# Kernel optimization log

Hardware: AMD Instinct MI355X
Metric: run time of the kernel (lower is better)

The kernel has to match this reference:

```python
import jax, jax.numpy as jnp
import numpy as np

B, T, RSS, L, FEAT, H = 256, 256, 12, 256, 8, 128
DIST_EPS = 1e-8
LN_EPS = 1e-5

def _lin(x, W, b):
    return x @ W.T + b

def setup_inputs() -> dict:
    key = jax.random.key(0)
    ks = jax.random.split(key, 20)
    w = lambda k, shape: jax.random.normal(k, shape, jnp.float32) * 0.1
    z = lambda *s: jnp.zeros(s, jnp.float32)
    # LED table: xyz positions in a room, frequency index in 1..12 (matches rss channels)
    pos = jax.random.uniform(ks[0], (L, 3), jnp.float32, 0.0, 5.0)
    freq = jax.random.randint(ks[1], (L,), 1, RSS + 1).astype(jnp.float32)
    return dict(
        rss_seq=jax.random.uniform(ks[2], (B, T, RSS), jnp.float32),
        global_led_pos_freq=jnp.concatenate([pos, freq[:, None]], axis=1),
        enc_W1=w(ks[3], (32, 4)), enc_b1=z(32), enc_W2=w(ks[4], (FEAT, 32)), enc_b2=z(FEAT),
        q_W1=w(ks[5], (64, 4)), q_b1=z(64), q_W2=w(ks[6], (64, 64)), q_b2=z(64),
        k_W1=w(ks[7], (64, FEAT + 3)), k_b1=z(64), k_W2=w(ks[8], (64, 64)), k_b2=z(64),
        Wih0=w(ks[9], (4 * H, RSS * (1 + FEAT))), Whh0=w(ks[10], (4 * H, H)), bih0=z(4 * H), bhh0=z(4 * H),
        Wih1=w(ks[11], (4 * H, H)), Whh1=w(ks[12], (4 * H, H)), bih1=z(4 * H), bhh1=z(4 * H),
        ln_g=jnp.ones((H,), jnp.float32), ln_b=z(H),
        fc_W1=w(ks[13], (H // 2, H)), fc_b1=z(H // 2), fc_W2=w(ks[14], (3, H // 2)), fc_b2=z(3),
    )

def _lstm_cell(x, h, c, Wih, Whh, bih, bhh):
    g = x @ Wih.T + bih + h @ Whh.T + bhh  # [B, 4H], pytorch gate order i,f,g,o
    i, f, gg, o = jnp.split(g, 4, axis=-1)
    c = jax.nn.sigmoid(f) * c + jax.nn.sigmoid(i) * jnp.tanh(gg)
    h = jax.nn.sigmoid(o) * jnp.tanh(c)
    return h, c

def _forward(rss_seq, global_led_pos_freq, enc_W1, enc_b1, enc_W2, enc_b2,
             q_W1, q_b1, q_W2, q_b2, k_W1, k_b1, k_W2, k_b2,
             Wih0, Whh0, bih0, bhh0, Wih1, Whh1, bih1, bhh1,
             ln_g, ln_b, fc_W1, fc_b1, fc_W2, fc_b2):
    batch, t_len, rss_dim = rss_seq.shape
    led_pos = global_led_pos_freq[:, :3]   # [L,3]
    led_freq = global_led_pos_freq[:, 3]   # [L]
    rss_freqs = jnp.arange(1, rss_dim + 1, dtype=rss_seq.dtype)
    freq_mask = rss_freqs[:, None] == led_freq[None, :]  # [RSS, L] bool
    # global LED features are a buffer computed under no_grad in torch
    led_feat = jax.lax.stop_gradient(
        jax.nn.relu(_lin(jax.nn.relu(_lin(global_led_pos_freq, enc_W1, enc_b1)), enc_W2, enc_b2)))  # [L,FEAT]
    keys = _lin(jax.nn.relu(_lin(jnp.concatenate([led_feat, led_pos], axis=1), k_W1, k_b1)), k_W2, k_b2)  # [L,64]
    neg = jnp.finfo(rss_seq.dtype).min

    def step(carry, rss_t):
        prev_pos, h0, c0, h1, c1 = carry  # prev_pos [B,3]
        q_in = jnp.concatenate(
            [rss_t[..., None], jnp.broadcast_to(prev_pos[:, None, :], (batch, rss_dim, 3))], axis=-1)  # [B,RSS,4]
        q = _lin(jax.nn.relu(_lin(q_in, q_W1, q_b1)), q_W2, q_b2)  # [B,RSS,64]
        scores = jnp.einsum('bqd,ld->bql', q, keys)  # [B,RSS,L]
        dist_sq = jnp.sum((prev_pos[:, None, :] - led_pos[None, :, :]) ** 2, axis=-1)  # [B,L]
        scores = scores + (-0.5 * jnp.log(dist_sq + DIST_EPS))[:, None, :]
        scores = jnp.where(freq_mask[None], scores, neg)
        attn = jax.nn.softmax(scores, axis=-1)
        agg = jnp.einsum('bql,lf->bqf', attn, led_feat)  # [B,RSS,FEAT]
        x = jnp.concatenate([rss_t[..., None], agg], axis=-1).reshape(batch, -1)  # [B, RSS*(1+FEAT)]
        h0n, c0n = _lstm_cell(x, h0, c0, Wih0, Whh0, bih0, bhh0)
        h1n, c1n = _lstm_cell(h0n, h1, c1, Wih1, Whh1, bih1, bhh1)
        y = h1n
        mu = jnp.mean(y, axis=-1, keepdims=True)
        var = jnp.var(y, axis=-1, keepdims=True)
        y = (y - mu) / jnp.sqrt(var + LN_EPS) * ln_g + ln_b
        pred = _lin(jax.nn.relu(_lin(y, fc_W1, fc_b1)), fc_W2, fc_b2)  # [B,3]
        return (pred, h0n, c0n, h1n, c1n), pred

    prev0 = jnp.broadcast_to(jnp.mean(led_pos, axis=0, keepdims=True), (batch, 3))
    hz = jnp.zeros((batch, Whh0.shape[1]), rss_seq.dtype)
    _, outs = jax.lax.scan(step, (prev0, hz, hz, hz, hz), jnp.swapaxes(rss_seq, 0, 1))
    return jnp.swapaxes(outs, 0, 1)  # [B,T,3]

def reference(rss_seq, global_led_pos_freq, enc_W1, enc_b1, enc_W2, enc_b2,
              q_W1, q_b1, q_W2, q_b2, k_W1, k_b1, k_W2, k_b2,
              Wih0, Whh0, bih0, bhh0, Wih1, Whh1, bih1, bhh1,
              ln_g, ln_b, fc_W1, fc_b1, fc_W2, fc_b2):
    return _forward(rss_seq, global_led_pos_freq, enc_W1, enc_b1, enc_W2, enc_b2,
                    q_W1, q_b1, q_W2, q_b2, k_W1, k_b1, k_W2, k_b2,
                    Wih0, Whh0, bih0, bhh0, Wih1, Whh1, bih1, bhh1,
                    ln_g, ln_b, fc_W1, fc_b1, fc_W2, fc_b2)
```

## Files before the change

kernel.cpp:

```cpp
#include <hip/hip_runtime.h>
#include <hip/hip_fp16.h>
#include <math.h>

#define B_ 256
#define T_ 256
#define RSS_ 12
#define L_ 256
#define FEAT_ 8
#define H_ 128

constexpr int OFF_PW0  = 0;
constexpr int OFF_PW1  = OFF_PW0 + 63488;
constexpr int OFF_W1L  = OFF_PW1 + 32768;
constexpr int OFF_B0   = OFF_W1L + 32768;
constexpr int OFF_B1   = OFF_B0 + 512;
constexpr int OFF_QW1T = OFF_B1 + 512;
constexpr int OFF_FC1  = OFF_QW1T + 256;
constexpr int OFF_K2T4 = OFF_FC1 + 8192;
constexpr int OFF_KB   = OFF_K2T4 + 16384;
constexpr int OFF_LF   = OFF_KB + 256;
constexpr int OFF_LPX  = OFF_LF + 2048;
constexpr int OFF_LPY  = OFF_LPX + 256;
constexpr int OFF_LPZ  = OFF_LPY + 256;
constexpr int OFF_MEAN = OFF_LPZ + 256;
constexpr int OFF_PREV0= OFF_MEAN + 8;
constexpr int OFF_INT  = OFF_PREV0 + 4;

__device__ __forceinline__ unsigned packh2(float a, float b) {
  const unsigned short lo = __half_as_ushort(__float2half(a));
  const unsigned short hi = __half_as_ushort(__float2half(b));
  return (unsigned)lo | ((unsigned)hi << 16);
}
__device__ __forceinline__ __half2 u2h2(unsigned u){ union { unsigned u; __half2 h; } c; c.u = u; return c.h; }
__device__ __forceinline__ float sigf(float x){ return 1.f/(1.f+expf(-x)); }

#if __has_builtin(__builtin_amdgcn_fdot2)
typedef _Float16 h2v __attribute__((ext_vector_type(2)));
__device__ __forceinline__ float d2(unsigned w, unsigned z, float acc) {
  union { unsigned u; h2v h; } cw, cz; cw.u = w; cz.u = z;
  return __builtin_amdgcn_fdot2(cw.h, cz.h, acc, false);
}
#else
__device__ __forceinline__ float d2(unsigned w, unsigned z, float acc) {
  const __half2 hw = u2h2(w), hz = u2h2(z);
  acc = fmaf(__low2float(hw),  __low2float(hz),  acc);
  return fmaf(__high2float(hw), __high2float(hz), acc);
}
#endif

constexpr int SZ_PW0 = 63488, SZ_PW1 = 32768, SZ_W1L = 32768, SZ_B = 512, SZ_Q = 256, SZ_FC = 8192;
constexpr int TOT_T = SZ_PW0 + SZ_PW1 + SZ_W1L + SZ_B + SZ_B + SZ_Q + SZ_FC;

__global__ void k_prep(const float* __restrict__ Wih0, const float* __restrict__ Whh0,
                       const float* __restrict__ bih0, const float* __restrict__ bhh0,
                       const float* __restrict__ Wih1, const float* __restrict__ Whh1,
                       const float* __restrict__ bih1, const float* __restrict__ bhh1,
                       const float* __restrict__ qW1,  const float* __restrict__ fcW1,
                       float* __restrict__ ws) {
  unsigned* wsu = (unsigned*)ws;
  for (int t = blockIdx.x*blockDim.x + threadIdx.x; t < TOT_T; t += gridDim.x*blockDim.x) {
    int u = t;
    if (u < SZ_PW0) {
      const int k = u & 3, j = (u >> 2) & 511, q = u >> 11;
      const int p = 4*q + k;
      float lo, hi;
      if (p < 60) {
        const int r = p / 5, e0 = 2*(p % 5), e1 = e0 + 1;
        lo = Wih0[j*108 + r*9 + e0];
        hi = (e1 <= 8) ? Wih0[j*108 + r*9 + e1] : 0.f;
      } else {
        const int i0 = 2*(p - 60);
        lo = Whh0[j*128 + i0]; hi = Whh0[j*128 + i0 + 1];
      }
      wsu[OFF_PW0 + u] = packh2(lo, hi); continue;
    } u -= SZ_PW0;
    if (u < SZ_PW1) {
      const int k = u & 3, j = (u >> 2) & 511, q = u >> 11;
      const int i0 = 2*(4*q + k);
      wsu[OFF_PW1 + u] = packh2(Wih1[j*128 + i0], Wih1[j*128 + i0 + 1]); continue;
    } u -= SZ_PW1;
    if (u < SZ_W1L) {
      const int k = u & 3, j = (u >> 2) & 511, q = u >> 11;
      const int i0 = 2*(4*q + k);
      wsu[OFF_W1L + u] = packh2(Whh1[j*128 + i0], Whh1[j*128 + i0 + 1]); continue;
    } u -= SZ_W1L;
    if (u < SZ_B) { ws[OFF_B0+u] = bih0[u]+bhh0[u]; continue; } u -= SZ_B;
    if (u < SZ_B) { ws[OFF_B1+u] = bih1[u]+bhh1[u]; continue; } u -= SZ_B;
    if (u < SZ_Q) { const int c=u>>6, j=u&63; ws[OFF_QW1T+u] = qW1[j*4+c]; continue; } u -= SZ_Q;
    { const int c = u >> 8, rem = u & 255, j = rem >> 2, k = rem & 3;
      ws[OFF_FC1 + u] = fcW1[j*128 + (c<<2) + k]; }
  }
}

__global__ __launch_bounds__(256) void k_led(const float* __restrict__ gplf,
    const float* __restrict__ encW1, const float* __restrict__ encb1,
    const float* __restrict__ encW2, const float* __restrict__ encb2,
    const float* __restrict__ kW1, const float* __restrict__ kb1,
    const float* __restrict__ kW2, const float* __restrict__ kb2,
    const float* __restrict__ qW2, const float* __restrict__ qb2,
    float* __restrict__ ws) {
  __shared__ float sLF[L_][FEAT_];
  __shared__ float sP[L_][3];
  __shared__ int   sR[L_];
  const int l = threadIdx.x;
  const float p0=gplf[l*4+0], p1=gplf[l*4+1], p2=gplf[l*4+2], fr=gplf[l*4+3];

  float e1[32];
  for (int j=0;j<32;++j) {
    float v = encb1[j] + encW1[j*4+0]*p0 + encW1[j*4+1]*p1 + encW1[j*4+2]*p2 + encW1[j*4+3]*fr;
    e1[j] = fmaxf(v,0.f);
  }
  float lf[8];
  for (int f=0;f<8;++f) {
    float v = encb2[f];
    for (int j=0;j<32;++j) v += encW2[f*32+j]*e1[j];
    lf[f] = fmaxf(v,0.f);
  }
  float kin[11] = {lf[0],lf[1],lf[2],lf[3],lf[4],lf[5],lf[6],lf[7],p0,p1,p2};
  float hh[64];
  for (int j=0;j<64;++j) {
    float v = kb1[j];
    for (int c=0;c<11;++c) v += kW1[j*11+c]*kin[c];
    hh[j]=fmaxf(v,0.f);
  }
  float kk[64];
  for (int d=0;d<64;++d) {
    float v = kb2[d];
    for (int j=0;j<64;++j) v += kW2[d*64+j]*hh[j];
    kk[d]=v;
  }
  float kbv=0.f;
  for (int d=0;d<64;++d) kbv += qb2[d]*kk[d];
  ws[OFF_KB+l]=kbv;
  for (int e=0;e<64;++e) {
    float acc=0.f;
    for (int d=0;d<64;++d) acc += qW2[d*64+e]*kk[d];
    ws[OFF_K2T4 + (e>>2)*1024 + l*4 + (e&3)] = acc;
  }
  for (int f=0;f<8;++f){ ws[OFF_LF+l*8+f]=lf[f]; sLF[l][f]=lf[f]; }
  ws[OFF_LPX+l]=p0; ws[OFF_LPY+l]=p1; ws[OFF_LPZ+l]=p2;
  sP[l][0]=p0; sP[l][1]=p1; sP[l][2]=p2;
  const int r = (int)fr - 1;
  sR[l]=r;
  int* iws = (int*)(ws + OFF_INT);
  iws[l] = r;
  __syncthreads();
  if (l==0) {
    int* cntp = iws + 256;
    int* idxp = cntp + 16;
    int c[12]; for (int r2=0;r2<12;++r2) c[r2]=0;
    for (int i=0;i<L_;++i){ int r2=sR[i]; idxp[r2*256 + c[r2]] = i; c[r2]++; }
    for (int r2=0;r2<12;++r2) cntp[r2]=c[r2];
    float mx=0.f,my=0.f,mz=0.f;
    for (int i=0;i<L_;++i){mx+=sP[i][0];my+=sP[i][1];mz+=sP[i][2];}
    ws[OFF_PREV0+0]=mx/(float)L_; ws[OFF_PREV0+1]=my/(float)L_; ws[OFF_PREV0+2]=mz/(float)L_;
    for (int f=0;f<8;++f){ float s=0.f; for (int i=0;i<L_;++i) s+=sLF[i][f]; ws[OFF_MEAN+f]=s/(float)L_; }
  }
}

__global__ __launch_bounds__(512,1) void k_main(const float* __restrict__ rss,
    const float* __restrict__ qb1, const float* __restrict__ lng, const float* __restrict__ lnb,
    const float* __restrict__ fcb1, const float* __restrict__ fcW2, const float* __restrict__ fcb2,
    const float* __restrict__ ws, float* __restrict__ out) {
  const int b = blockIdx.x, tid = threadIdx.x;
  const int lane = tid & 63, wave = tid >> 6;
  const int j = tid;

  __shared__ uint4 sW1L[8192];
  __shared__ unsigned sLFh[1024];
  __shared__ float sLPx[256], sLPy[256], sLPz[256];
  __shared__ float sKB[256];
  __shared__ float sQ[256], sqb1v[64];
  __shared__ float sLNG[128], sLNB[128];
  __shared__ float sfcb1[64], sfcW2v[192], sfcb2v[4];
  __shared__ float sMEANv[8];
  __shared__ __align__(16) unsigned sz0h[124];
  __shared__ __align__(16) unsigned sz1h[128];
  __shared__ float sc0[128], sc1[128];
  __shared__ __align__(16) float sa[12][68];
  __shared__ float ssv[256];
  __shared__ float sg[512];
  __shared__ __align__(16) float syv[128];
  __shared__ float sprev[4];
  __shared__ int   sledR[256], scnt[16];
  __shared__ unsigned short sidx16[12*256];

  const uint4* PW0 = (const uint4*)((const unsigned*)ws + OFF_PW0);
  const uint4* PW1 = (const uint4*)((const unsigned*)ws + OFF_PW1);
#define LW0(Q) const uint4 w0_##Q = PW0[Q*512 + j];
#define LW1(Q) const uint4 w1_##Q = PW1[Q*512 + j];
  LW0(0) LW0(1) LW0(2) LW0(3) LW0(4) LW0(5) LW0(6) LW0(7) LW0(8) LW0(9)
  LW0(10) LW0(11) LW0(12) LW0(13) LW0(14) LW0(15) LW0(16) LW0(17) LW0(18) LW0(19)
  LW0(20) LW0(21) LW0(22) LW0(23) LW0(24) LW0(25) LW0(26) LW0(27) LW0(28) LW0(29) LW0(30)
  LW1(0) LW1(1) LW1(2) LW1(3) LW1(4) LW1(5) LW1(6) LW1(7)
  LW1(8) LW1(9) LW1(10) LW1(11) LW1(12) LW1(13) LW1(14) LW1(15)
  const float biasA = ws[OFF_B0 + j];
  const float biasB = ws[OFF_B1 + j];

  {
    const uint4* W1Lg = (const uint4*)((const unsigned*)ws + OFF_W1L);
    for (int u = tid; u < 8192; u += 512) sW1L[u] = W1Lg[u];
    for (int u = tid; u < 1024; u += 512) sLFh[u] = packh2(ws[OFF_LF+2*u], ws[OFF_LF+2*u+1]);
  }
  if (tid < 256) { sLPx[tid]=ws[OFF_LPX+tid]; sLPy[tid]=ws[OFF_LPY+tid]; sLPz[tid]=ws[OFF_LPZ+tid];
                   sKB[tid]=ws[OFF_KB+tid]; sQ[tid]=ws[OFF_QW1T+tid]; }
  if (tid < 64) { sqb1v[tid]=qb1[tid]; sfcb1[tid]=fcb1[tid]; }
  if (tid < 128){ sLNG[tid]=lng[tid]; sLNB[tid]=lnb[tid]; sc0[tid]=0.f; sc1[tid]=0.f; sz1h[tid]=0u; }
  if (tid < 192) sfcW2v[tid]=fcW2[tid];
  if (tid < 3)  { sfcb2v[tid]=fcb2[tid]; sprev[tid]=ws[OFF_PREV0+tid]; }
  if (tid < 8)   sMEANv[tid]=ws[OFF_MEAN+tid];
  if (tid < 64)  sz0h[60+tid]=0u;
  {
    const int* iws = (const int*)(ws + OFF_INT);
    if (tid < 256) sledR[tid]=iws[tid];
    if (tid < 12)  scnt[tid]=iws[256+tid];
    for (int u = tid; u < 12*256; u += 512) sidx16[u] = (unsigned short)iws[272+u];
  }
  __syncthreads();

  const float* rb = rss + (size_t)b*T_*12;
  float x0 = rb[wave];
  float x1 = (wave < 4) ? rb[wave+8] : 0.f;

  const float4* K2g = (const float4*)(ws + OFF_K2T4);
  const float4* F1g = (const float4*)(ws + OFF_FC1);
  const uint4*  z0u4 = (const uint4*)sz0h;
  const uint4*  z1u4 = (const uint4*)sz1h;

  for (int t = 0; t < T_; ++t) {
    float xn0 = 0.f, xn1 = 0.f;
    if (t+1 < T_) {
      xn0 = rb[(t+1)*12 + wave];
      if (wave < 4) xn1 = rb[(t+1)*12 + wave+8];
    }
    const float px = sprev[0], py = sprev[1], pz = sprev[2];

    {
      float v = sqb1v[lane] + x0*sQ[lane] + px*sQ[64+lane] + py*sQ[128+lane] + pz*sQ[192+lane];
      sa[wave][lane] = fmaxf(v, 0.f);
      if (wave < 4) {
        float v2 = sqb1v[lane] + x1*sQ[lane] + px*sQ[64+lane] + py*sQ[128+lane] + pz*sQ[192+lane];
        sa[wave+8][lane] = fmaxf(v2, 0.f);
      }
    }
    __syncthreads();

    if (tid < 256) {
      const int l = tid, r = sledR[l];
      float a0 = sKB[l], a1 = 0.f;
      const float4* ar4 = (const float4*)&sa[r][0];
      #pragma unroll 1
      for (int cc = 0; cc < 4; ++cc) {
        const float4 wA = K2g[(cc*4+0)*256 + l];
        const float4 wB = K2g[(cc*4+1)*256 + l];
        const float4 wC = K2g[(cc*4+2)*256 + l];
        const float4 wD = K2g[(cc*4+3)*256 + l];
        const float4 aA = ar4[cc*4+0], aB = ar4[cc*4+1], aC = ar4[cc*4+2], aD = ar4[cc*4+3];
        a0=fmaf(aA.x,wA.x,a0); a1=fmaf(aA.y,wA.y,a1); a0=fmaf(aA.z,wA.z,a0); a1=fmaf(aA.w,wA.w,a1);
        a0=fmaf(aB.x,wB.x,a0); a1=fmaf(aB.y,wB.y,a1); a0=fmaf(aB.z,wB.z,a0); a1=fmaf(aB.w,wB.w,a1);
        a0=fmaf(aC.x,wC.x,a0); a1=fmaf(aC.y,wC.y,a1); a0=fmaf(aC.z,wC.z,a0); a1=fmaf(aC.w,wC.w,a1);
        a0=fmaf(aD.x,wD.x,a0); a1=fmaf(aD.y,wD.y,a1); a0=fmaf(aD.z,wD.z,a0); a1=fmaf(aD.w,wD.w,a1);
      }
      const float dx = px-sLPx[tid], dy = py-sLPy[tid], dz = pz-sLPz[tid];
      ssv[tid] = a0 + a1 - 0.5f*logf(dx*dx+dy*dy+dz*dz + 1e-8f);
    }
    __syncthreads();

    for (int rr = 0; rr < 2; ++rr) {
      if (rr == 1 && wave >= 4) break;
      const int r = wave + rr*8;
      const int cnt = scnt[r];
      float vmax = -3.402823466e38f;
      for (int c = lane; c < cnt; c += 64) vmax = fmaxf(vmax, ssv[sidx16[r*256+c]]);
      #pragma unroll
      for (int o = 32; o > 0; o >>= 1) vmax = fmaxf(vmax, __shfl_xor(vmax, o));
      float ps=0.f, p0=0.f,p1=0.f,p2=0.f,p3=0.f,p4=0.f,p5=0.f,p6=0.f,p7=0.f;
      for (int c = lane; c < cnt; c += 64) {
        const int li = sidx16[r*256+c];
        const float p = expf(ssv[li]-vmax);
        ps += p;
        const unsigned* lf = sLFh + li*4;
        const __half2 A=u2h2(lf[0]), Bq=u2h2(lf[1]), C=u2h2(lf[2]), D=u2h2(lf[3]);
        p0 += p*__low2float(A); p1 += p*__high2float(A);
        p2 += p*__low2float(Bq); p3 += p*__high2float(Bq);
        p4 += p*__low2float(C); p5 += p*__high2float(C);
        p6 += p*__low2float(D); p7 += p*__high2float(D);
      }
      #pragma unroll
      for (int o = 32; o > 0; o >>= 1) {
        ps += __shfl_xor(ps,o);
        p0 += __shfl_xor(p0,o); p1 += __shfl_xor(p1,o);
        p2 += __shfl_xor(p2,o); p3 += __shfl_xor(p3,o);
        p4 += __shfl_xor(p4,o); p5 += __shfl_xor(p5,o);
        p6 += __shfl_xor(p6,o); p7 += __shfl_xor(p7,o);
      }
      if (lane == 0) {
        const float xv = rr ? x1 : x0;
        float a0v,a1v,a2v,a3v,a4v,a5v,a6v,a7v;
        if (cnt > 0) {
          const float inv = 1.f/ps;
          a0v=p0*inv; a1v=p1*inv; a2v=p2*inv; a3v=p3*inv;
          a4v=p4*inv; a5v=p5*inv; a6v=p6*inv; a7v=p7*inv;
        } else {
          a0v=sMEANv[0]; a1v=sMEANv[1]; a2v=sMEANv[2]; a3v=sMEANv[3];
          a4v=sMEANv[4]; a5v=sMEANv[5]; a6v=sMEANv[6]; a7v=sMEANv[7];
        }
        sz0h[r*5+0] = packh2(xv,  a0v);
        sz0h[r*5+1] = packh2(a1v, a2v);
        sz0h[r*5+2] = packh2(a3v, a4v);
        sz0h[r*5+3] = packh2(a5v, a6v);
        sz0h[r*5+4] = packh2(a7v, 0.f);
      }
    }
    __syncthreads();

    {
      float g0 = biasA, g1 = 0.f, g2 = 0.f, g3 = 0.f;
#define D0(Q) { const uint4 Z = z0u4[Q]; \
      g0 = d2(w0_##Q.x, Z.x, g0); g1 = d2(w0_##Q.y, Z.y, g1); \
      g2 = d2(w0_##Q.z, Z.z, g2); g3 = d2(w0_##Q.w, Z.w, g3); }
      D0(0) D0(1) D0(2) D0(3) D0(4) D0(5) D0(6) D0(7) D0(8) D0(9)
      D0(10) D0(11) D0(12) D0(13) D0(14) D0(15) D0(16) D0(17) D0(18) D0(19)
      D0(20) D0(21) D0(22) D0(23) D0(24) D0(25) D0(26) D0(27) D0(28) D0(29) D0(30)
      sg[j] = (g0+g1)+(g2+g3);
    }
    __syncthreads();

    if (tid < 64) {
      const int v = tid;
      const float iA=sigf(sg[2*v]),     iB=sigf(sg[2*v+1]);
      const float fA=sigf(sg[128+2*v]), fB=sigf(sg[128+2*v+1]);
      const float gA=tanhf(sg[256+2*v]),gB=tanhf(sg[256+2*v+1]);
      const float oA=sigf(sg[384+2*v]), oB=sigf(sg[384+2*v+1]);
      const float cA = fA*sc0[2*v]   + iA*gA;
      const float cB = fB*sc0[2*v+1] + iB*gB;
      sc0[2*v] = cA; sc0[2*v+1] = cB;
      const float hA = oA*tanhf(cA), hB = oB*tanhf(cB);
      const unsigned hp = packh2(hA, hB);
      sz0h[60+v] = hp; sz1h[v] = hp;
    }
    __syncthreads();

    {
      float g0 = biasB, g1 = 0.f, g2 = 0.f, g3 = 0.f;
#define E1(Q) { const uint4 Z = z1u4[Q]; \
      g0 = d2(w1_##Q.x, Z.x, g0); g1 = d2(w1_##Q.y, Z.y, g1); \
      g2 = d2(w1_##Q.z, Z.z, g2); g3 = d2(w1_##Q.w, Z.w, g3); }
      E1(0) E1(1) E1(2) E1(3) E1(4) E1(5) E1(6) E1(7)
      E1(8) E1(9) E1(10) E1(11) E1(12) E1(13) E1(14) E1(15)
      #pragma unroll 4
      for (int q = 0; q < 16; ++q) {
        const uint4 W = sW1L[q*512 + j];
        const uint4 Z = z1u4[16+q];
        g0 = d2(W.x, Z.x, g0); g1 = d2(W.y, Z.y, g1);
        g2 = d2(W.z, Z.z, g2); g3 = d2(W.w, Z.w, g3);
      }
      sg[j] = (g0+g1)+(g2+g3);
    }
    __syncthreads();

    if (tid < 64) {
      const int v = tid;
      const float iA=sigf(sg[2*v]),     iB=sigf(sg[2*v+1]);
      const float fA=sigf(sg[128+2*v]), fB=sigf(sg[128+2*v+1]);
      const float gA=tanhf(sg[256+2*v]),gB=tanhf(sg[256+2*v+1]);
      const float oA=sigf(sg[384+2*v]), oB=sigf(sg[384+2*v+1]);
      const float cA = fA*sc1[2*v]   + iA*gA;
      const float cB = fB*sc1[2*v+1] + iB*gB;
      sc1[2*v] = cA; sc1[2*v+1] = cB;
      const float hA = oA*tanhf(cA), hB = oB*tanhf(cB);
      sz1h[64+v] = packh2(hA, hB);
      float s = hA + hB, qs = hA*hA + hB*hB;
      #pragma unroll
      for (int o = 32; o > 0; o >>= 1) { s += __shfl_xor(s,o); qs += __shfl_xor(qs,o); }
      const float mu = s*(1.f/128.f);
      const float rs = 1.f/sqrtf(qs*(1.f/128.f) - mu*mu + 1e-5f);
      const float yA = (hA-mu)*rs*sLNG[2*v] + sLNB[2*v];
      const float yB = (hB-mu)*rs*sLNG[2*v+1] + sLNB[2*v+1];
      syv[2*v] = yA; syv[2*v+1] = yB;
      float acc = sfcb1[v], acc2 = 0.f;
      const float4* sy4 = (const float4*)syv;
      #pragma unroll 1
      for (int cc = 0; cc < 8; ++cc) {
        const float4 wA = F1g[(cc*4+0)*64 + v];
        const float4 wB = F1g[(cc*4+1)*64 + v];
        const float4 wC = F1g[(cc*4+2)*64 + v];
        const float4 wD = F1g[(cc*4+3)*64 + v];
        const float4 zA = sy4[cc*4+0], zB = sy4[cc*4+1], zC = sy4[cc*4+2], zD = sy4[cc*4+3];
        acc=fmaf(wA.x,zA.x,acc); acc2=fmaf(wA.y,zA.y,acc2); acc=fmaf(wA.z,zA.z,acc); acc2=fmaf(wA.w,zA.w,acc2);
        acc=fmaf(wB.x,zB.x,acc); acc2=fmaf(wB.y,zB.y,acc2); acc=fmaf(wB.z,zB.z,acc); acc2=fmaf(wB.w,zB.w,acc2);
        acc=fmaf(wC.x,zC.x,acc); acc2=fmaf(wC.y,zC.y,acc2); acc=fmaf(wC.z,zC.z,acc); acc2=fmaf(wC.w,zC.w,acc2);
        acc=fmaf(wD.x,zD.x,acc); acc2=fmaf(wD.y,zD.y,acc2); acc=fmaf(wD.z,zD.z,acc); acc2=fmaf(wD.w,zD.w,acc2);
      }
      const float f1 = fmaxf(acc+acc2, 0.f);
      float a0 = sfcW2v[v]*f1, a1 = sfcW2v[64+v]*f1, a2 = sfcW2v[128+v]*f1;
      #pragma unroll
      for (int o = 32; o > 0; o >>= 1) {
        a0 += __shfl_xor(a0,o); a1 += __shfl_xor(a1,o); a2 += __shfl_xor(a2,o);
      }
      if (v < 3) {
        const float r = (v==0 ? a0 : (v==1 ? a1 : a2)) + sfcb2v[v];
        out[((size_t)b*T_+t)*3+v] = r;
        sprev[v] = r;
      }
    }
    __syncthreads();

    x0 = xn0; x1 = xn1;
  }
}

extern "C" void kernel_launch(void* const* d_in, const int* in_sizes, int n_in,
                              void* d_out, int out_size, void* d_ws, size_t ws_size,
                              hipStream_t stream) {
  const float* rss   = (const float*)d_in[0];
  const float* gplf  = (const float*)d_in[1];
  const float* encW1 = (const float*)d_in[2];
  const float* encb1 = (const float*)d_in[3];
  const float* encW2 = (const float*)d_in[4];
  const float* encb2 = (const float*)d_in[5];
  const float* qW1   = (const float*)d_in[6];
  const float* qb1   = (const float*)d_in[7];
  const float* qW2   = (const float*)d_in[8];
  const float* qb2   = (const float*)d_in[9];
  const float* kW1   = (const float*)d_in[10];
  const float* kb1   = (const float*)d_in[11];
  const float* kW2   = (const float*)d_in[12];
  const float* kb2   = (const float*)d_in[13];
  const float* Wih0  = (const float*)d_in[14];
  const float* Whh0  = (const float*)d_in[15];
  const float* bih0  = (const float*)d_in[16];
  const float* bhh0  = (const float*)d_in[17];
  const float* Wih1  = (const float*)d_in[18];
  const float* Whh1  = (const float*)d_in[19];
  const float* bih1  = (const float*)d_in[20];
  const float* bhh1  = (const float*)d_in[21];
  const float* lng   = (const float*)d_in[22];
  const float* lnb   = (const float*)d_in[23];
  const float* fcW1  = (const float*)d_in[24];
  const float* fcb1  = (const float*)d_in[25];
  const float* fcW2  = (const float*)d_in[26];
  const float* fcb2  = (const float*)d_in[27];
  float* ws   = (float*)d_ws;
  float* outp = (float*)d_out;

  hipLaunchKernelGGL(k_prep, dim3(256), dim3(256), 0, stream,
                     Wih0,Whh0,bih0,bhh0,Wih1,Whh1,bih1,bhh1,qW1,fcW1,ws);
  hipLaunchKernelGGL(k_led, dim3(1), dim3(256), 0, stream,
                     gplf,encW1,encb1,encW2,encb2,kW1,kb1,kW2,kb2,qW2,qb2,ws);
  hipLaunchKernelGGL(k_main, dim3(B_), dim3(512), 0, stream,
                     rss,qb1,lng,lnb,fcb1,fcW2,fcb2,ws,outp);
}
```

Baseline: 2.589 ms.

## Stream layer-0 weights from memory and spread K-proj and gate work across threads

Layer-0 LSTM input weights are no longer held in 31 uint4 registers per thread. They are re-read from global memory through the cache on every timestep, which frees a large block of VGPRs. The LED key projection now uses all 512 threads, each pair splitting the 16 float4 chunks and combining partial sums with a shuffle. The layer-0 gate nonlinearity now uses 128 threads, one hidden unit each, packed to half2 via shuffle. The intent is lower register pressure and more parallelism per step, at the cost of extra memory or cache traffic for the weights inside the serial time loop.

```diff
diff --git a/kernel.cpp b/kernel.cpp
--- a/kernel.cpp
+++ b/kernel.cpp
@@ -187,11 +187,7 @@
 
   const uint4* PW0 = (const uint4*)((const unsigned*)ws + OFF_PW0);
   const uint4* PW1 = (const uint4*)((const unsigned*)ws + OFF_PW1);
-#define LW0(Q) const uint4 w0_##Q = PW0[Q*512 + j];
 #define LW1(Q) const uint4 w1_##Q = PW1[Q*512 + j];
-  LW0(0) LW0(1) LW0(2) LW0(3) LW0(4) LW0(5) LW0(6) LW0(7) LW0(8) LW0(9)
-  LW0(10) LW0(11) LW0(12) LW0(13) LW0(14) LW0(15) LW0(16) LW0(17) LW0(18) LW0(19)
-  LW0(20) LW0(21) LW0(22) LW0(23) LW0(24) LW0(25) LW0(26) LW0(27) LW0(28) LW0(29) LW0(30)
   LW1(0) LW1(1) LW1(2) LW1(3) LW1(4) LW1(5) LW1(6) LW1(7)
   LW1(8) LW1(9) LW1(10) LW1(11) LW1(12) LW1(13) LW1(14) LW1(15)
   const float biasA = ws[OFF_B0 + j];
@@ -245,24 +241,25 @@
     }
     __syncthreads();
 
-    if (tid < 256) {
-      const int l = tid, r = sledR[l];
-      float a0 = sKB[l], a1 = 0.f;
+    {
+      const int l = tid >> 1, k = tid & 1;
+      const int r = sledR[l];
       const float4* ar4 = (const float4*)&sa[r][0];
-      #pragma unroll 1
-      for (int cc = 0; cc < 4; ++cc) {
-        const float4 wA = K2g[(cc*4+0)*256 + l];
-        const float4 wB = K2g[(cc*4+1)*256 + l];
-        const float4 wC = K2g[(cc*4+2)*256 + l];
-        const float4 wD = K2g[(cc*4+3)*256 + l];
-        const float4 aA = ar4[cc*4+0], aB = ar4[cc*4+1], aC = ar4[cc*4+2], aD = ar4[cc*4+3];
-        a0=fmaf(aA.x,wA.x,a0); a1=fmaf(aA.y,wA.y,a1); a0=fmaf(aA.z,wA.z,a0); a1=fmaf(aA.w,wA.w,a1);
-        a0=fmaf(aB.x,wB.x,a0); a1=fmaf(aB.y,wB.y,a1); a0=fmaf(aB.z,wB.z,a0); a1=fmaf(aB.w,wB.w,a1);
-        a0=fmaf(aC.x,wC.x,a0); a1=fmaf(aC.y,wC.y,a1); a0=fmaf(aC.z,wC.z,a0); a1=fmaf(aC.w,wC.w,a1);
-        a0=fmaf(aD.x,wD.x,a0); a1=fmaf(aD.y,wD.y,a1); a0=fmaf(aD.z,wD.z,a0); a1=fmaf(aD.w,wD.w,a1);
-      }
-      const float dx = px-sLPx[tid], dy = py-sLPy[tid], dz = pz-sLPz[tid];
-      ssv[tid] = a0 + a1 - 0.5f*logf(dx*dx+dy*dy+dz*dz + 1e-8f);
+      float a0 = 0.f, a1 = 0.f;
+      #pragma unroll
+      for (int c2 = 0; c2 < 8; ++c2) {
+        const int cc = k*8 + c2;
+        const float4 w = K2g[cc*256 + l];
+        const float4 a = ar4[cc];
+        a0 = fmaf(a.x, w.x, a0); a1 = fmaf(a.y, w.y, a1);
+        a0 = fmaf(a.z, w.z, a0); a1 = fmaf(a.w, w.w, a1);
+      }
+      float s = a0 + a1;
+      s += __shfl_xor(s, 1);
+      if (k == 0) {
+        const float dx = px-sLPx[l], dy = py-sLPy[l], dz = pz-sLPz[l];
+        ssv[l] = s + sKB[l] - 0.5f*logf(dx*dx+dy*dy+dz*dz + 1e-8f);
+      }
     }
     __syncthreads();
 
@@ -316,28 +313,30 @@
 
     {
       float g0 = biasA, g1 = 0.f, g2 = 0.f, g3 = 0.f;
-#define D0(Q) { const uint4 Z = z0u4[Q]; \
-      g0 = d2(w0_##Q.x, Z.x, g0); g1 = d2(w0_##Q.y, Z.y, g1); \
-      g2 = d2(w0_##Q.z, Z.z, g2); g3 = d2(w0_##Q.w, Z.w, g3); }
-      D0(0) D0(1) D0(2) D0(3) D0(4) D0(5) D0(6) D0(7) D0(8) D0(9)
-      D0(10) D0(11) D0(12) D0(13) D0(14) D0(15) D0(16) D0(17) D0(18) D0(19)
-      D0(20) D0(21) D0(22) D0(23) D0(24) D0(25) D0(26) D0(27) D0(28) D0(29) D0(30)
+      const uint4* wp = PW0 + j;
+      #pragma unroll
+      for (int q = 0; q < 31; ++q) {
+        const uint4 W = wp[q*512];
+        const uint4 Z = z0u4[q];
+        g0 = d2(W.x, Z.x, g0); g1 = d2(W.y, Z.y, g1);
+        g2 = d2(W.z, Z.z, g2); g3 = d2(W.w, Z.w, g3);
+      }
       sg[j] = (g0+g1)+(g2+g3);
     }
     __syncthreads();
 
-    if (tid < 64) {
+    if (tid < 128) {
       const int v = tid;
-      const float iA=sigf(sg[2*v]),     iB=sigf(sg[2*v+1]);
-      const float fA=sigf(sg[128+2*v]), fB=sigf(sg[128+2*v+1]);
-      const float gA=tanhf(sg[256+2*v]),gB=tanhf(sg[256+2*v+1]);
-      const float oA=sigf(sg[384+2*v]), oB=sigf(sg[384+2*v+1]);
-      const float cA = fA*sc0[2*v]   + iA*gA;
-      const float cB = fB*sc0[2*v+1] + iB*gB;
-      sc0[2*v] = cA; sc0[2*v+1] = cB;
-      const float hA = oA*tanhf(cA), hB = oB*tanhf(cB);
-      const unsigned hp = packh2(hA, hB);
-      sz0h[60+v] = hp; sz1h[v] = hp;
+      const float gi = sigf(sg[v]),      gf = sigf(sg[128+v]);
+      const float gg = tanhf(sg[256+v]), go = sigf(sg[384+v]);
+      const float c = gf*sc0[v] + gi*gg;
+      sc0[v] = c;
+      const float hh = go*tanhf(c);
+      const float hn = __shfl_down(hh, 1);
+      if (!(v & 1)) {
+        const unsigned hp = packh2(hh, hn);
+        sz0h[60+(v>>1)] = hp; sz1h[v>>1] = hp;
+      }
     }
     __syncthreads();
 
```

New measurement: 3.289 ms. 1.27x slower.

## Stream layer-0 input weights from global and overlap recurrent dot with attention stages

Applied to the files above, without the earlier changes.

The layer-0 gate weights are no longer held in registers for the whole loop. Each step reloads them from global memory (L2/cache) in chunks and interleaves the recurrent h0 part of the dot product (chunks 15-30) with the query, key and softmax stages that come before the input part is ready. This frees many registers and hides the layer-0 recurrent matmul behind the attention work. In exchange it adds global loads every timestep. __syncthreads is also replaced by a barrier that waits only on LDS (lgkmcnt) and not on outstanding global loads.

```diff
diff --git a/kernel.cpp b/kernel.cpp
--- a/kernel.cpp
+++ b/kernel.cpp
@@ -36,17 +36,23 @@
 
 #if __has_builtin(__builtin_amdgcn_fdot2)
 typedef _Float16 h2v __attribute__((ext_vector_type(2)));
-__device__ __forceinline__ float d2(unsigned w, unsigned z, float acc) {
+__device__ __forceinline__ float d2f(unsigned w, unsigned z, float acc) {
   union { unsigned u; h2v h; } cw, cz; cw.u = w; cz.u = z;
   return __builtin_amdgcn_fdot2(cw.h, cz.h, acc, false);
 }
 #else
-__device__ __forceinline__ float d2(unsigned w, unsigned z, float acc) {
+__device__ __forceinline__ float d2f(unsigned w, unsigned z, float acc) {
   const __half2 hw = u2h2(w), hz = u2h2(z);
   acc = fmaf(__low2float(hw),  __low2float(hz),  acc);
   return fmaf(__high2float(hw), __high2float(hz), acc);
 }
 #endif
+
+__device__ __forceinline__ void bar_lds() {
+  asm volatile("s_waitcnt lgkmcnt(0)" ::: "memory");
+  __builtin_amdgcn_s_barrier();
+  asm volatile("" ::: "memory");
+}
 
 constexpr int SZ_PW0 = 63488, SZ_PW1 = 32768, SZ_W1L = 32768, SZ_B = 512, SZ_Q = 256, SZ_FC = 8192;
 constexpr int TOT_T = SZ_PW0 + SZ_PW1 + SZ_W1L + SZ_B + SZ_B + SZ_Q + SZ_FC;
@@ -185,20 +191,17 @@
   __shared__ int   sledR[256], scnt[16];
   __shared__ unsigned short sidx16[12*256];
 
-  const uint4* PW0 = (const uint4*)((const unsigned*)ws + OFF_PW0);
-  const uint4* PW1 = (const uint4*)((const unsigned*)ws + OFF_PW1);
-#define LW0(Q) const uint4 w0_##Q = PW0[Q*512 + j];
+  const unsigned* wsu = (const unsigned*)ws;
+  const uint4* PW0 = (const uint4*)(wsu + OFF_PW0);
+  const uint4* PW1 = (const uint4*)(wsu + OFF_PW1);
 #define LW1(Q) const uint4 w1_##Q = PW1[Q*512 + j];
-  LW0(0) LW0(1) LW0(2) LW0(3) LW0(4) LW0(5) LW0(6) LW0(7) LW0(8) LW0(9)
-  LW0(10) LW0(11) LW0(12) LW0(13) LW0(14) LW0(15) LW0(16) LW0(17) LW0(18) LW0(19)
-  LW0(20) LW0(21) LW0(22) LW0(23) LW0(24) LW0(25) LW0(26) LW0(27) LW0(28) LW0(29) LW0(30)
   LW1(0) LW1(1) LW1(2) LW1(3) LW1(4) LW1(5) LW1(6) LW1(7)
   LW1(8) LW1(9) LW1(10) LW1(11) LW1(12) LW1(13) LW1(14) LW1(15)
   const float biasA = ws[OFF_B0 + j];
   const float biasB = ws[OFF_B1 + j];
 
   {
-    const uint4* W1Lg = (const uint4*)((const unsigned*)ws + OFF_W1L);
+    const uint4* W1Lg = (const uint4*)(wsu + OFF_W1L);
     for (int u = tid; u < 8192; u += 512) sW1L[u] = W1Lg[u];
     for (int u = tid; u < 1024; u += 512) sLFh[u] = packh2(ws[OFF_LF+2*u], ws[OFF_LF+2*u+1]);
   }
@@ -226,6 +229,11 @@
   const float4* F1g = (const float4*)(ws + OFF_FC1);
   const uint4*  z0u4 = (const uint4*)sz0h;
   const uint4*  z1u4 = (const uint4*)sz1h;
+  const uint4*  wp0 = PW0 + j;
+
+#define CONSA(V, Q) { const uint4 Z = z0u4[Q]; \
+    gA0 = d2f(V.x, Z.x, gA0); gA1 = d2f(V.y, Z.y, gA1); \
+    gA2 = d2f(V.z, Z.z, gA2); gA3 = d2f(V.w, Z.w, gA3); }
 
   for (int t = 0; t < T_; ++t) {
     float xn0 = 0.f, xn1 = 0.f;
@@ -234,6 +242,10 @@
       if (wave < 4) xn1 = rb[(t+1)*12 + wave+8];
     }
     const float px = sprev[0], py = sprev[1], pz = sprev[2];
+
+    float gA0 = biasA, gA1 = 0.f, gA2 = 0.f, gA3 = 0.f;
+    uint4 c15 = wp0[15*512], c16 = wp0[16*512], c17 = wp0[17*512];
+    uint4 c18 = wp0[18*512], c19 = wp0[19*512], c20 = wp0[20*512];
 
     {
       float v = sqb1v[lane] + x0*sQ[lane] + px*sQ[64+lane] + py*sQ[128+lane] + pz*sQ[192+lane];
@@ -243,7 +255,10 @@
         sa[wave+8][lane] = fmaxf(v2, 0.f);
       }
     }
-    __syncthreads();
+    CONSA(c15,15) CONSA(c16,16) CONSA(c17,17) CONSA(c18,18) CONSA(c19,19) CONSA(c20,20)
+    uint4 c21 = wp0[21*512], c22 = wp0[22*512], c23 = wp0[23*512];
+    uint4 c24 = wp0[24*512], c25 = wp0[25*512], c26 = wp0[26*512];
+    bar_lds();
 
     if (tid < 256) {
       const int l = tid, r = sledR[l];
@@ -264,67 +279,71 @@
       const float dx = px-sLPx[tid], dy = py-sLPy[tid], dz = pz-sLPz[tid];
       ssv[tid] = a0 + a1 - 0.5f*logf(dx*dx+dy*dy+dz*dz + 1e-8f);
     }
-    __syncthreads();
+    CONSA(c21,21) CONSA(c22,22) CONSA(c23,23) CONSA(c24,24) CONSA(c25,25) CONSA(c26,26)
+    uint4 c27 = wp0[27*512], c28 = wp0[28*512], c29 = wp0[29*512], c30 = wp0[30*512];
+    bar_lds();
 
     for (int rr = 0; rr < 2; ++rr) {
-      if (rr == 1 && wave >= 4) break;
-      const int r = wave + rr*8;
-      const int cnt = scnt[r];
-      float vmax = -3.402823466e38f;
-      for (int c = lane; c < cnt; c += 64) vmax = fmaxf(vmax, ssv[sidx16[r*256+c]]);
+      if (!(rr == 1 && wave >= 4)) {
+        const int r = wave + rr*8;
+        const int cnt = scnt[r];
+        float vmax = -3.402823466e38f;
+        for (int c = lane; c < cnt; c += 64) vmax = fmaxf(vmax, ssv[sidx16[r*256+c]]);
+        #pragma unroll
+        for (int o = 32; o > 0; o >>= 1) vmax = fmaxf(vmax, __shfl_xor(vmax, o));
+        float ps=0.f, p0=0.f,p1=0.f,p2=0.f,p3=0.f,p4=0.f,p5=0.f,p6=0.f,p7=0.f;
+        for (int c = lane; c < cnt; c += 64) {
+          const int li = sidx16[r*256+c];
+          const float p = expf(ssv[li]-vmax);
+          ps += p;
+          const unsigned* lf = sLFh + li*4;
+          const __half2 A=u2h2(lf[0]), Bq=u2h2(lf[1]), C=u2h2(lf[2]), D=u2h2(lf[3]);
+          p0 += p*__low2float(A); p1 += p*__high2float(A);
+          p2 += p*__low2float(Bq); p3 += p*__high2float(Bq);
+          p4 += p*__low2float(C); p5 += p*__high2float(C);
+          p6 += p*__low2float(D); p7 += p*__high2float(D);
+        }
+        #pragma unroll
+        for (int o = 32; o > 0; o >>= 1) {
+          ps += __shfl_xor(ps,o);
+          p0 += __shfl_xor(p0,o); p1 += __shfl_xor(p1,o);
+          p2 += __shfl_xor(p2,o); p3 += __shfl_xor(p3,o);
+          p4 += __shfl_xor(p4,o); p5 += __shfl_xor(p5,o);
+          p6 += __shfl_xor(p6,o); p7 += __shfl_xor(p7,o);
+        }
+        if (lane == 0) {
+          const float xv = rr ? x1 : x0;
+          float a0v,a1v,a2v,a3v,a4v,a5v,a6v,a7v;
+          if (cnt > 0) {
+            const float inv = 1.f/ps;
+            a0v=p0*inv; a1v=p1*inv; a2v=p2*inv; a3v=p3*inv;
+            a4v=p4*inv; a5v=p5*inv; a6v=p6*inv; a7v=p7*inv;
+          } else {
+            a0v=sMEANv[0]; a1v=sMEANv[1]; a2v=sMEANv[2]; a3v=sMEANv[3];
+            a4v=sMEANv[4]; a5v=sMEANv[5]; a6v=sMEANv[6]; a7v=sMEANv[7];
+          }
+          sz0h[r*5+0] = packh2(xv,  a0v);
+          sz0h[r*5+1] = packh2(a1v, a2v);
+          sz0h[r*5+2] = packh2(a3v, a4v);
+          sz0h[r*5+3] = packh2(a5v, a6v);
+          sz0h[r*5+4] = packh2(a7v, 0.f);
+        }
+      }
+    }
+    CONSA(c27,27) CONSA(c28,28) CONSA(c29,29) CONSA(c30,30)
+    bar_lds();
+
+    {
       #pragma unroll
-      for (int o = 32; o > 0; o >>= 1) vmax = fmaxf(vmax, __shfl_xor(vmax, o));
-      float ps=0.f, p0=0.f,p1=0.f,p2=0.f,p3=0.f,p4=0.f,p5=0.f,p6=0.f,p7=0.f;
-      for (int c = lane; c < cnt; c += 64) {
-        const int li = sidx16[r*256+c];
-        const float p = expf(ssv[li]-vmax);
-        ps += p;
-        const unsigned* lf = sLFh + li*4;
-        const __half2 A=u2h2(lf[0]), Bq=u2h2(lf[1]), C=u2h2(lf[2]), D=u2h2(lf[3]);
-        p0 += p*__low2float(A); p1 += p*__high2float(A);
-        p2 += p*__low2float(Bq); p3 += p*__high2float(Bq);
-        p4 += p*__low2float(C); p5 += p*__high2float(C);
-        p6 += p*__low2float(D); p7 += p*__high2float(D);
-      }
-      #pragma unroll
-      for (int o = 32; o > 0; o >>= 1) {
-        ps += __shfl_xor(ps,o);
-        p0 += __shfl_xor(p0,o); p1 += __shfl_xor(p1,o);
-        p2 += __shfl_xor(p2,o); p3 += __shfl_xor(p3,o);
-        p4 += __shfl_xor(p4,o); p5 += __shfl_xor(p5,o);
-        p6 += __shfl_xor(p6,o); p7 += __shfl_xor(p7,o);
-      }
-      if (lane == 0) {
-        const float xv = rr ? x1 : x0;
-        float a0v,a1v,a2v,a3v,a4v,a5v,a6v,a7v;
-        if (cnt > 0) {
-          const float inv = 1.f/ps;
-          a0v=p0*inv; a1v=p1*inv; a2v=p2*inv; a3v=p3*inv;
-          a4v=p4*inv; a5v=p5*inv; a6v=p6*inv; a7v=p7*inv;
-        } else {
-          a0v=sMEANv[0]; a1v=sMEANv[1]; a2v=sMEANv[2]; a3v=sMEANv[3];
-          a4v=sMEANv[4]; a5v=sMEANv[5]; a6v=sMEANv[6]; a7v=sMEANv[7];
-        }
-        sz0h[r*5+0] = packh2(xv,  a0v);
-        sz0h[r*5+1] = packh2(a1v, a2v);
-        sz0h[r*5+2] = packh2(a3v, a4v);
-        sz0h[r*5+3] = packh2(a5v, a6v);
-        sz0h[r*5+4] = packh2(a7v, 0.f);
-      }
-    }
-    __syncthreads();
-
-    {
-      float g0 = biasA, g1 = 0.f, g2 = 0.f, g3 = 0.f;
-#define D0(Q) { const uint4 Z = z0u4[Q]; \
-      g0 = d2(w0_##Q.x, Z.x, g0); g1 = d2(w0_##Q.y, Z.y, g1); \
-      g2 = d2(w0_##Q.z, Z.z, g2); g3 = d2(w0_##Q.w, Z.w, g3); }
-      D0(0) D0(1) D0(2) D0(3) D0(4) D0(5) D0(6) D0(7) D0(8) D0(9)
-      D0(10) D0(11) D0(12) D0(13) D0(14) D0(15) D0(16) D0(17) D0(18) D0(19)
-      D0(20) D0(21) D0(22) D0(23) D0(24) D0(25) D0(26) D0(27) D0(28) D0(29) D0(30)
-      sg[j] = (g0+g1)+(g2+g3);
-    }
-    __syncthreads();
+      for (int q = 0; q < 15; ++q) {
+        const uint4 W = wp0[q*512];
+        const uint4 Z = z0u4[q];
+        gA0 = d2f(W.x, Z.x, gA0); gA1 = d2f(W.y, Z.y, gA1);
+        gA2 = d2f(W.z, Z.z, gA2); gA3 = d2f(W.w, Z.w, gA3);
+      }
+      sg[j] = (gA0+gA1)+(gA2+gA3);
+    }
+    bar_lds();
 
     if (tid < 64) {
       const int v = tid;
@@ -339,25 +358,25 @@
       const unsigned hp = packh2(hA, hB);
       sz0h[60+v] = hp; sz1h[v] = hp;
     }
-    __syncthreads();
+    bar_lds();
 
     {
       float g0 = biasB, g1 = 0.f, g2 = 0.f, g3 = 0.f;
 #define E1(Q) { const uint4 Z = z1u4[Q]; \
-      g0 = d2(w1_##Q.x, Z.x, g0); g1 = d2(w1_##Q.y, Z.y, g1); \
-      g2 = d2(w1_##Q.z, Z.z, g2); g3 = d2(w1_##Q.w, Z.w, g3); }
+      g0 = d2f(w1_##Q.x, Z.x, g0); g1 = d2f(w1_##Q.y, Z.y, g1); \
+      g2 = d2f(w1_##Q.z, Z.z, g2); g3 = d2f(w1_##Q.w, Z.w, g3); }
       E1(0) E1(1) E1(2) E1(3) E1(4) E1(5) E1(6) E1(7)
       E1(8) E1(9) E1(10) E1(11) E1(12) E1(13) E1(14) E1(15)
       #pragma unroll 4
       for (int q = 0; q < 16; ++q) {
         const uint4 W = sW1L[q*512 + j];
         const uint4 Z = z1u4[16+q];
-        g0 = d2(W.x, Z.x, g0); g1 = d2(W.y, Z.y, g1);
-        g2 = d2(W.z, Z.z, g2); g3 = d2(W.w, Z.w, g3);
+        g0 = d2f(W.x, Z.x, g0); g1 = d2f(W.y, Z.y, g1);
+        g2 = d2f(W.z, Z.z, g2); g3 = d2f(W.w, Z.w, g3);
       }
       sg[j] = (g0+g1)+(g2+g3);
     }
-    __syncthreads();
+    bar_lds();
 
     if (tid < 64) {
       const int v = tid;
@@ -404,7 +423,7 @@
         sprev[v] = r;
       }
     }
-    __syncthreads();
+    bar_lds();
 
     x0 = xn0; x1 = xn1;
   }
```

Result: slower. 3.099 ms (+19.7%).
